# Kernel tuning notes

Hardware: AMD Instinct MI355X
Metric: run time of the kernel (lower is better)

Reference implementation:

```python
import jax, jax.numpy as jnp
import numpy as np

TOP_K = 2

def setup_inputs() -> dict:
    key = jax.random.key(0)
    ks = jax.random.split(key, 6)
    B, T, D, H, E = 4, 2048, 1024, 4096, 8
    s = 0.02
    return {
        "x": jax.random.normal(ks[0], (B, T, D), dtype=jnp.float32),
        "Wg": jax.random.normal(ks[1], (E, D), dtype=jnp.float32) * s,
        "W1": jax.random.normal(ks[2], (E, H, D), dtype=jnp.float32) * s,
        "b1": jax.random.normal(ks[3], (E, H), dtype=jnp.float32) * s,
        "W2": jax.random.normal(ks[4], (E, D, H), dtype=jnp.float32) * s,
        "b2": jax.random.normal(ks[5], (E, D), dtype=jnp.float32) * s,
    }

def reference(x, Wg, W1, b1, W2, b2):
    B, T, D = x.shape
    N = B * T
    xf = x.reshape(N, D)
    # Gate: logits (N, E), top-k indices + softmax weights over top-k logits
    logits = jnp.einsum("nd,ed->ne", xf, Wg)
    top_logits, top_idx = jax.lax.top_k(logits, TOP_K)            # (N, K)
    top_w = jax.nn.softmax(top_logits, axis=-1)                   # (N, K)
    # Dense all-expert MLP (faithful to original: every expert on every token)
    h = jax.nn.gelu(jnp.einsum("nd,ehd->neh", xf, W1) + b1[None], approximate=False)  # (N, E, H)
    all_out = jnp.einsum("neh,edh->ned", h, W2) + b2[None]        # (N, E, D)
    # Gather top-k expert outputs per token and combine
    selected = jnp.take_along_axis(all_out, top_idx[:, :, None], axis=1)  # (N, K, D)
    out = jnp.sum(selected * top_w[:, :, None], axis=1)           # (N, D)
    return out.reshape(B, T, D)
```

## Files before the change

### kernel.cpp

```cpp
#include <hip/hip_runtime.h>
#include <cstdint>
#include <cstddef>

#define N_TOK 8192
#define D_DIM 1024
#define H_DIM 4096
#define E_NUM 8
#define BM 128
#define BN 128
#define BK 32

typedef __bf16 bf16x8 __attribute__((ext_vector_type(8)));
typedef float floatx4 __attribute__((ext_vector_type(4)));
typedef unsigned short u16;

__device__ __forceinline__ u16 f2bf(float f) {
  unsigned int u = __float_as_uint(f);
  u += 0x7fff + ((u >> 16) & 1);
  return (u16)(u >> 16);
}

__device__ __forceinline__ void gload_lds16(const void* g, void* l) {
  __builtin_amdgcn_global_load_lds((const __attribute__((address_space(1))) void*)g,
                                   (__attribute__((address_space(3))) void*)l, 16, 0, 0);
}

__global__ void init_k(int* __restrict__ cnt) {
  if (threadIdx.x < E_NUM) cnt[threadIdx.x] = 0;
}

__global__ __launch_bounds__(256) void cvt_k(const float* __restrict__ s, u16* __restrict__ d) {
  size_t i = (size_t)blockIdx.x * 256 + threadIdx.x;
  float4 v = ((const float4*)s)[i];
  ushort4 o;
  o.x = f2bf(v.x); o.y = f2bf(v.y); o.z = f2bf(v.z); o.w = f2bf(v.w);
  ((ushort4*)d)[i] = o;
}

__global__ __launch_bounds__(256) void gate_k(const float* __restrict__ x,
                                              const float* __restrict__ Wg,
                                              const float* __restrict__ b2,
                                              float* __restrict__ out,
                                              int* __restrict__ cnt,
                                              int* __restrict__ rows,
                                              float* __restrict__ wrow) {
  int tid = threadIdx.x;
  int wv = tid >> 6, lane = tid & 63;
  int n = blockIdx.x * 4 + wv;
  const float* xr = x + (size_t)n * D_DIM;
  float acc[E_NUM];
#pragma unroll
  for (int e = 0; e < E_NUM; e++) acc[e] = 0.f;
#pragma unroll
  for (int q = 0; q < 4; q++) {
    int d = q * 256 + lane * 4;
    float4 xv = *(const float4*)(xr + d);
#pragma unroll
    for (int e = 0; e < E_NUM; e++) {
      float4 w4 = *(const float4*)(Wg + (size_t)e * D_DIM + d);
      acc[e] += xv.x * w4.x + xv.y * w4.y + xv.z * w4.z + xv.w * w4.w;
    }
  }
#pragma unroll
  for (int e = 0; e < E_NUM; e++) {
#pragma unroll
    for (int off = 32; off >= 1; off >>= 1) acc[e] += __shfl_xor(acc[e], off, 64);
  }
  int e0 = 0; float v0 = acc[0];
#pragma unroll
  for (int e = 1; e < E_NUM; e++) if (acc[e] > v0) { v0 = acc[e]; e0 = e; }
  int e1 = (e0 == 0) ? 1 : 0; float v1 = acc[e1];
#pragma unroll
  for (int e = 0; e < E_NUM; e++) if (e != e0 && acc[e] > v1) { v1 = acc[e]; e1 = e; }
  float p1 = expf(v1 - v0);
  float w0 = 1.f / (1.f + p1);
  float w1 = p1 / (1.f + p1);
  const float* b2a = b2 + (size_t)e0 * D_DIM;
  const float* b2b = b2 + (size_t)e1 * D_DIM;
  float* orow = out + (size_t)n * D_DIM;
#pragma unroll
  for (int q = 0; q < 4; q++) {
    int d = q * 256 + lane * 4;
    float4 a4 = *(const float4*)(b2a + d);
    float4 c4 = *(const float4*)(b2b + d);
    float4 o;
    o.x = w0 * a4.x + w1 * c4.x;
    o.y = w0 * a4.y + w1 * c4.y;
    o.z = w0 * a4.z + w1 * c4.z;
    o.w = w0 * a4.w + w1 * c4.w;
    *(float4*)(orow + d) = o;
  }
  if (lane == 0) {
    int p = atomicAdd(&cnt[e0], 1);
    rows[e0 * N_TOK + p] = n * 2;
    p = atomicAdd(&cnt[e1], 1);
    rows[e1 * N_TOK + p] = n * 2 + 1;
    wrow[n * 2] = w0;
    wrow[n * 2 + 1] = w1;
  }
}

__global__ __launch_bounds__(256) void fc1_k(const u16* __restrict__ xbf,
                                             const u16* __restrict__ w1bf,
                                             const float* __restrict__ b1,
                                             u16* __restrict__ hbf,
                                             const int* __restrict__ cnt,
                                             const int* __restrict__ rows) {
  int bx = blockIdx.x;
  int e = bx >> 11;
  int t = bx & 2047;
  int m0 = (t >> 5) * BM;
  int n0 = (t & 31) * BN;
  int ce = cnt[e];
  if (m0 >= ce) return;

  __shared__ __align__(16) u16 As[BM * BK];
  __shared__ __align__(16) u16 Bs[BN * BK];
  __shared__ int rows_s[BM];

  int tid = threadIdx.x;
  int wv = tid >> 6, lane = tid & 63;
  const int* erows = rows + e * N_TOK;
  if (tid < BM) {
    int p = m0 + tid;
    rows_s[tid] = (p < ce) ? erows[p] : 0;
  }
  int r4 = tid >> 2;
  int cb = (tid & 3) * 16;
  int pa0 = m0 + r4, pa1 = m0 + 64 + r4;
  int rid0 = (pa0 < ce) ? erows[pa0] : 0;
  int rid1 = (pa1 < ce) ? erows[pa1] : 0;
  const char* aptr0 = (const char*)(xbf + (size_t)(rid0 >> 1) * D_DIM) + cb;
  const char* aptr1 = (const char*)(xbf + (size_t)(rid1 >> 1) * D_DIM) + cb;
  const char* bptr = (const char*)(w1bf + ((size_t)e * H_DIM + n0 + r4) * D_DIM) + cb;
  u16* As_w = As + wv * 512;
  u16* Bs_w = Bs + wv * 512;

  floatx4 zero = {0.f, 0.f, 0.f, 0.f};
  floatx4 acc[4][4];
#pragma unroll
  for (int i = 0; i < 4; i++)
#pragma unroll
    for (int j = 0; j < 4; j++) acc[i][j] = zero;

  int wm = (wv >> 1) * 64;
  int wn = (wv & 1) * 64;
  int lrow = lane & 15;
  int lko = (lane >> 4) * 8;

  for (int kk = 0; kk < D_DIM / BK; kk++) {
    size_t koff = (size_t)kk * (BK * 2);
    __syncthreads();
    gload_lds16(aptr0 + koff, As_w);
    gload_lds16(aptr1 + koff, As_w + 2048);
    gload_lds16(bptr + koff, Bs_w);
    gload_lds16(bptr + (size_t)64 * D_DIM * 2 + koff, Bs_w + 2048);
    __syncthreads();
    bf16x8 a[4], b[4];
#pragma unroll
    for (int i = 0; i < 4; i++) a[i] = *(const bf16x8*)&As[(wm + i * 16 + lrow) * BK + lko];
#pragma unroll
    for (int j = 0; j < 4; j++) b[j] = *(const bf16x8*)&Bs[(wn + j * 16 + lrow) * BK + lko];
#pragma unroll
    for (int i = 0; i < 4; i++)
#pragma unroll
      for (int j = 0; j < 4; j++)
        acc[i][j] = __builtin_amdgcn_mfma_f32_16x16x32_bf16(a[i], b[j], acc[i][j], 0, 0, 0);
  }

  const float* b1e = b1 + (size_t)e * H_DIM + n0;
#pragma unroll
  for (int i = 0; i < 4; i++) {
#pragma unroll
    for (int j = 0; j < 4; j++) {
#pragma unroll
      for (int r = 0; r < 4; r++) {
        int ml = wm + i * 16 + (lane >> 4) * 4 + r;
        int nl = wn + j * 16 + (lane & 15);
        int p = m0 + ml;
        if (p < ce) {
          float v = acc[i][j][r] + b1e[nl];
          v = 0.5f * v * (1.0f + erff(v * 0.70710678118654752f));
          hbf[(size_t)rows_s[ml] * H_DIM + n0 + nl] = f2bf(v);
        }
      }
    }
  }
}

__global__ __launch_bounds__(256) void fc2_k(const u16* __restrict__ hbf,
                                             const u16* __restrict__ w2bf,
                                             float* __restrict__ out,
                                             const int* __restrict__ cnt,
                                             const int* __restrict__ rows,
                                             const float* __restrict__ wrow) {
  int bx = blockIdx.x;
  int e = bx >> 9;
  int t = bx & 511;
  int m0 = (t >> 3) * BM;
  int n0 = (t & 7) * BN;
  int ce = cnt[e];
  if (m0 >= ce) return;

  __shared__ __align__(16) u16 As[BM * BK];
  __shared__ __align__(16) u16 Bs[BN * BK];
  __shared__ int rows_s[BM];
  __shared__ float w_s[BM];

  int tid = threadIdx.x;
  int wv = tid >> 6, lane = tid & 63;
  const int* erows = rows + e * N_TOK;
  if (tid < BM) {
    int p = m0 + tid;
    int rid = (p < ce) ? erows[p] : 0;
    rows_s[tid] = rid;
    w_s[tid] = (p < ce) ? wrow[rid] : 0.f;
  }
  int r4 = tid >> 2;
  int cb = (tid & 3) * 16;
  int pa0 = m0 + r4, pa1 = m0 + 64 + r4;
  int rid0 = (pa0 < ce) ? erows[pa0] : 0;
  int rid1 = (pa1 < ce) ? erows[pa1] : 0;
  const char* aptr0 = (const char*)(hbf + (size_t)rid0 * H_DIM) + cb;
  const char* aptr1 = (const char*)(hbf + (size_t)rid1 * H_DIM) + cb;
  const char* bptr = (const char*)(w2bf + ((size_t)e * D_DIM + n0 + r4) * H_DIM) + cb;
  u16* As_w = As + wv * 512;
  u16* Bs_w = Bs + wv * 512;

  floatx4 zero = {0.f, 0.f, 0.f, 0.f};
  floatx4 acc[4][4];
#pragma unroll
  for (int i = 0; i < 4; i++)
#pragma unroll
    for (int j = 0; j < 4; j++) acc[i][j] = zero;

  int wm = (wv >> 1) * 64;
  int wn = (wv & 1) * 64;
  int lrow = lane & 15;
  int lko = (lane >> 4) * 8;

  for (int kk = 0; kk < H_DIM / BK; kk++) {
    size_t koff = (size_t)kk * (BK * 2);
    __syncthreads();
    gload_lds16(aptr0 + koff, As_w);
    gload_lds16(aptr1 + koff, As_w + 2048);
    gload_lds16(bptr + koff, Bs_w);
    gload_lds16(bptr + (size_t)64 * H_DIM * 2 + koff, Bs_w + 2048);
    __syncthreads();
    bf16x8 a[4], b[4];
#pragma unroll
    for (int i = 0; i < 4; i++) a[i] = *(const bf16x8*)&As[(wm + i * 16 + lrow) * BK + lko];
#pragma unroll
    for (int j = 0; j < 4; j++) b[j] = *(const bf16x8*)&Bs[(wn + j * 16 + lrow) * BK + lko];
#pragma unroll
    for (int i = 0; i < 4; i++)
#pragma unroll
      for (int j = 0; j < 4; j++)
        acc[i][j] = __builtin_amdgcn_mfma_f32_16x16x32_bf16(a[i], b[j], acc[i][j], 0, 0, 0);
  }

#pragma unroll
  for (int i = 0; i < 4; i++) {
#pragma unroll
    for (int j = 0; j < 4; j++) {
#pragma unroll
      for (int r = 0; r < 4; r++) {
        int ml = wm + i * 16 + (lane >> 4) * 4 + r;
        int nl = wn + j * 16 + (lane & 15);
        int p = m0 + ml;
        if (p < ce) {
          float v = acc[i][j][r] * w_s[ml];
          unsafeAtomicAdd(&out[(size_t)(rows_s[ml] >> 1) * D_DIM + n0 + nl], v);
        }
      }
    }
  }
}

extern "C" void kernel_launch(void* const* d_in, const int* in_sizes, int n_in,
                              void* d_out, int out_size, void* d_ws, size_t ws_size,
                              hipStream_t stream) {
  const float* x  = (const float*)d_in[0];
  const float* Wg = (const float*)d_in[1];
  const float* W1 = (const float*)d_in[2];
  const float* b1 = (const float*)d_in[3];
  const float* W2 = (const float*)d_in[4];
  const float* b2 = (const float*)d_in[5];
  float* out = (float*)d_out;

  char* ws = (char*)d_ws;
  size_t off = 0;
  auto alloc = [&](size_t bytes) -> void* {
    void* p = ws + off;
    off += (bytes + 255) & ~(size_t)255;
    return p;
  };
  int*   cnt  = (int*)alloc(E_NUM * sizeof(int));
  int*   rows = (int*)alloc((size_t)E_NUM * N_TOK * sizeof(int));
  float* wrow = (float*)alloc((size_t)N_TOK * 2 * sizeof(float));
  u16*   xbf  = (u16*)alloc((size_t)N_TOK * D_DIM * 2);
  u16*   w1bf = (u16*)alloc((size_t)E_NUM * H_DIM * D_DIM * 2);
  u16*   w2bf = (u16*)alloc((size_t)E_NUM * D_DIM * H_DIM * 2);
  u16*   hbf  = (u16*)alloc((size_t)N_TOK * 2 * H_DIM * 2);
  if (off > ws_size) return;

  init_k<<<1, 64, 0, stream>>>(cnt);
  cvt_k<<<(N_TOK * D_DIM) / 1024, 256, 0, stream>>>(x, xbf);
  cvt_k<<<(E_NUM * H_DIM * D_DIM) / 1024, 256, 0, stream>>>(W1, w1bf);
  cvt_k<<<(E_NUM * D_DIM * H_DIM) / 1024, 256, 0, stream>>>(W2, w2bf);
  gate_k<<<N_TOK / 4, 256, 0, stream>>>(x, Wg, b2, out, cnt, rows, wrow);
  fc1_k<<<E_NUM * 64 * 32, 256, 0, stream>>>(xbf, w1bf, b1, hbf, cnt, rows);
  fc2_k<<<E_NUM * 64 * 8, 256, 0, stream>>>(hbf, w2bf, out, cnt, rows, wrow);
}
```

Baseline: 1.057 ms.

## Swizzle LDS tiles, fuse x bf16 conversion into gate, use tanh GELU

Applies an XOR swizzle to the K-chunk column offset in the LDS tiles of both GEMMs, so fragment reads hit fewer bank conflicts. Folds the x-to-bf16 conversion into the gate kernel and drops one launch and one pass over x. Replaces the exact erf GELU with a tanh-style approximation built on __expf, and hoists the bias loads in the epilogues. The GELU approximation changes numerics against the reference's exact GELU, and the swizzle relies on the load and read mappings staying consistent.

```diff
diff --git a/kernel.cpp b/kernel.cpp
--- a/kernel.cpp
+++ b/kernel.cpp
@@ -20,6 +20,11 @@
   return (u16)(u >> 16);
 }
 
+__device__ __forceinline__ float gelu_f(float v) {
+  float y = v * (0.7978845608f + 0.0356774081f * v * v);
+  return v / (1.0f + __expf(-2.0f * y));
+}
+
 __device__ __forceinline__ void gload_lds16(const void* g, void* l) {
   __builtin_amdgcn_global_load_lds((const __attribute__((address_space(1))) void*)g,
                                    (__attribute__((address_space(3))) void*)l, 16, 0, 0);
@@ -43,7 +48,8 @@
                                               float* __restrict__ out,
                                               int* __restrict__ cnt,
                                               int* __restrict__ rows,
-                                              float* __restrict__ wrow) {
+                                              float* __restrict__ wrow,
+                                              u16* __restrict__ xbf) {
   int tid = threadIdx.x;
   int wv = tid >> 6, lane = tid & 63;
   int n = blockIdx.x * 4 + wv;
@@ -55,6 +61,9 @@
   for (int q = 0; q < 4; q++) {
     int d = q * 256 + lane * 4;
     float4 xv = *(const float4*)(xr + d);
+    ushort4 xo;
+    xo.x = f2bf(xv.x); xo.y = f2bf(xv.y); xo.z = f2bf(xv.z); xo.w = f2bf(xv.w);
+    *(ushort4*)(xbf + (size_t)n * D_DIM + d) = xo;
 #pragma unroll
     for (int e = 0; e < E_NUM; e++) {
       float4 w4 = *(const float4*)(Wg + (size_t)e * D_DIM + d);
@@ -126,7 +135,7 @@
     rows_s[tid] = (p < ce) ? erows[p] : 0;
   }
   int r4 = tid >> 2;
-  int cb = (tid & 3) * 16;
+  int cb = ((tid & 3) ^ ((r4 >> 1) & 3)) * 16;
   int pa0 = m0 + r4, pa1 = m0 + 64 + r4;
   int rid0 = (pa0 < ce) ? erows[pa0] : 0;
   int rid1 = (pa1 < ce) ? erows[pa1] : 0;
@@ -146,7 +155,7 @@
   int wm = (wv >> 1) * 64;
   int wn = (wv & 1) * 64;
   int lrow = lane & 15;
-  int lko = (lane >> 4) * 8;
+  int lko = ((lane >> 4) ^ ((lrow >> 1) & 3)) * 8;
 
   for (int kk = 0; kk < D_DIM / BK; kk++) {
     size_t koff = (size_t)kk * (BK * 2);
@@ -169,19 +178,21 @@
   }
 
   const float* b1e = b1 + (size_t)e * H_DIM + n0;
+  float bias[4];
+#pragma unroll
+  for (int j = 0; j < 4; j++) bias[j] = b1e[wn + j * 16 + (lane & 15)];
 #pragma unroll
   for (int i = 0; i < 4; i++) {
-#pragma unroll
-    for (int j = 0; j < 4; j++) {
-#pragma unroll
-      for (int r = 0; r < 4; r++) {
-        int ml = wm + i * 16 + (lane >> 4) * 4 + r;
-        int nl = wn + j * 16 + (lane & 15);
-        int p = m0 + ml;
-        if (p < ce) {
-          float v = acc[i][j][r] + b1e[nl];
-          v = 0.5f * v * (1.0f + erff(v * 0.70710678118654752f));
-          hbf[(size_t)rows_s[ml] * H_DIM + n0 + nl] = f2bf(v);
+    int mlb = wm + i * 16 + (lane >> 4) * 4;
+#pragma unroll
+    for (int r = 0; r < 4; r++) {
+      int ml = mlb + r;
+      if (m0 + ml < ce) {
+        size_t rowoff = (size_t)rows_s[ml] * H_DIM + n0 + wn + (lane & 15);
+#pragma unroll
+        for (int j = 0; j < 4; j++) {
+          float v = acc[i][j][r] + bias[j];
+          hbf[rowoff + j * 16] = f2bf(gelu_f(v));
         }
       }
     }
@@ -217,7 +228,7 @@
     w_s[tid] = (p < ce) ? wrow[rid] : 0.f;
   }
   int r4 = tid >> 2;
-  int cb = (tid & 3) * 16;
+  int cb = ((tid & 3) ^ ((r4 >> 1) & 3)) * 16;
   int pa0 = m0 + r4, pa1 = m0 + 64 + r4;
   int rid0 = (pa0 < ce) ? erows[pa0] : 0;
   int rid1 = (pa1 < ce) ? erows[pa1] : 0;
@@ -237,7 +248,7 @@
   int wm = (wv >> 1) * 64;
   int wn = (wv & 1) * 64;
   int lrow = lane & 15;
-  int lko = (lane >> 4) * 8;
+  int lko = ((lane >> 4) ^ ((lrow >> 1) & 3)) * 8;
 
   for (int kk = 0; kk < H_DIM / BK; kk++) {
     size_t koff = (size_t)kk * (BK * 2);
@@ -261,16 +272,16 @@
 
 #pragma unroll
   for (int i = 0; i < 4; i++) {
-#pragma unroll
-    for (int j = 0; j < 4; j++) {
-#pragma unroll
-      for (int r = 0; r < 4; r++) {
-        int ml = wm + i * 16 + (lane >> 4) * 4 + r;
-        int nl = wn + j * 16 + (lane & 15);
-        int p = m0 + ml;
-        if (p < ce) {
-          float v = acc[i][j][r] * w_s[ml];
-          unsafeAtomicAdd(&out[(size_t)(rows_s[ml] >> 1) * D_DIM + n0 + nl], v);
+    int mlb = wm + i * 16 + (lane >> 4) * 4;
+#pragma unroll
+    for (int r = 0; r < 4; r++) {
+      int ml = mlb + r;
+      if (m0 + ml < ce) {
+        float wsc = w_s[ml];
+        float* orow = out + (size_t)(rows_s[ml] >> 1) * D_DIM + n0 + wn + (lane & 15);
+#pragma unroll
+        for (int j = 0; j < 4; j++) {
+          unsafeAtomicAdd(&orow[j * 16], acc[i][j][r] * wsc);
         }
       }
     }
@@ -305,10 +316,9 @@
   if (off > ws_size) return;
 
   init_k<<<1, 64, 0, stream>>>(cnt);
-  cvt_k<<<(N_TOK * D_DIM) / 1024, 256, 0, stream>>>(x, xbf);
   cvt_k<<<(E_NUM * H_DIM * D_DIM) / 1024, 256, 0, stream>>>(W1, w1bf);
   cvt_k<<<(E_NUM * D_DIM * H_DIM) / 1024, 256, 0, stream>>>(W2, w2bf);
-  gate_k<<<N_TOK / 4, 256, 0, stream>>>(x, Wg, b2, out, cnt, rows, wrow);
+  gate_k<<<N_TOK / 4, 256, 0, stream>>>(x, Wg, b2, out, cnt, rows, wrow, xbf);
   fc1_k<<<E_NUM * 64 * 32, 256, 0, stream>>>(xbf, w1bf, b1, hbf, cnt, rows);
   fc2_k<<<E_NUM * 64 * 8, 256, 0, stream>>>(hbf, w2bf, out, cnt, rows, wrow);
 }
```

Result: faster. 959.2 us (-9.3%).
